# Kernel tuning notes

Hardware: AMD Instinct MI355X
Metric: run time of the kernel (lower is better)

## Reference

```python
import jax, jax.numpy as jnp
import numpy as np

S = 8192   # seq_len (== max_seq_len)
K = 4096   # in_features
N = 4096   # out_features


def setup_inputs() -> dict:
    key = jax.random.key(0)
    k1, k2, k3, k4, k5 = jax.random.split(key, 5)
    # symmetric int8 activations and weights in [-127, 127]
    x = jax.random.randint(k1, (S, K), -127, 128, dtype=jnp.int32).astype(jnp.int8)
    weight_q = jax.random.randint(k2, (N, K), -127, 128, dtype=jnp.int32).astype(jnp.int8)
    # positive dequant scales (per-row symmetric quant: scale = absmax/127)
    scale_x = jax.random.uniform(k3, (S,), minval=0.5, maxval=2.0, dtype=jnp.float32) / 127.0
    scale_w = jax.random.uniform(k4, (N,), minval=0.5, maxval=2.0, dtype=jnp.float32) / 127.0
    # per-output-row requantization scale from the MinMax observer
    scale_y = jax.random.uniform(k5, (S,), minval=0.5, maxval=2.0, dtype=jnp.float32)
    return {"x": x, "weight_q": weight_q, "scale_x": scale_x,
            "scale_w": scale_w, "scale_y": scale_y}


def reference(x, weight_q, scale_x, scale_w, scale_y):
    # int8 GEMM with int32 accumulation: acc[s, n] = sum_k x[s, k] * w[n, k]
    acc = jnp.matmul(x.astype(jnp.int32), weight_q.T.astype(jnp.int32))  # [S, N] int32
    # fused three-scale dequant + requant: (acc * sx[s] * sw[n]) / sy[s]
    scale = (scale_x / scale_y)[:, None] * scale_w[None, :]               # [S, N]
    out_f = acc.astype(jnp.float32) * scale
    out_q = jnp.clip(jnp.round(out_f), -128.0, 127.0).astype(jnp.int8)    # int8 output
    return out_q, scale_y
```

## Files before the change

kernel.cpp:

```cpp
#include <hip/hip_runtime.h>
#include <stdint.h>

#define S_DIM 8192
#define K_DIM 4096
#define N_DIM 4096

#define BM 128
#define BN 128
#define BK 128

typedef int v4i __attribute__((ext_vector_type(4)));

__global__ void pack_i8(const int* __restrict__ src, int* __restrict__ dst,
                        int n4) {
    int i = blockIdx.x * blockDim.x + threadIdx.x;
    if (i >= n4) return;
    int4 a = ((const int4*)src)[i];
    dst[i] = (a.x & 0xFF) | ((a.y & 0xFF) << 8) | ((a.z & 0xFF) << 16)
           | ((a.w & 0xFF) << 24);
}

__global__ void copy_sy(const float* __restrict__ sy, float* __restrict__ out) {
    int i = blockIdx.x * blockDim.x + threadIdx.x;
    if (i < S_DIM) out[(size_t)S_DIM * N_DIM + i] = sy[i];
}

__device__ __forceinline__ void g2lds16(const void* g, void* l) {
    __builtin_amdgcn_global_load_lds((const __attribute__((address_space(1))) void*)g,
                                     (__attribute__((address_space(3))) void*)l,
                                     16, 0, 0);
}

__launch_bounds__(256)
__global__ void gemm_i8(const signed char* __restrict__ xp,
                        const signed char* __restrict__ wp,
                        const float* __restrict__ sx,
                        const float* __restrict__ sw,
                        const float* __restrict__ sy,
                        float* __restrict__ out) {
    __shared__ __align__(16) signed char As[BM * BK];
    __shared__ __align__(16) signed char Bs[BN * BK];

    const int tid  = threadIdx.x;
    const int lane = tid & 63;
    const int quad = lane >> 4;
    const int l16  = lane & 15;
    const int wave = tid >> 6;
    const int wm = wave >> 1;
    const int wn = wave & 1;
    const int bn = blockIdx.x;
    const int bm = blockIdx.y;

    const signed char* aG = xp + (size_t)(bm * BM) * K_DIM;
    const signed char* bG = wp + (size_t)(bn * BN) * K_DIM;

    const int csw = l16 & 7;

    v4i acc[4][4];
#pragma unroll
    for (int i = 0; i < 4; i++)
#pragma unroll
        for (int j = 0; j < 4; j++) acc[i][j] = 0;

    for (int kk = 0; kk < K_DIM; kk += BK) {
        __syncthreads();
#pragma unroll
        for (int i = 0; i < 4; i++) {
            int li  = i * 256 + tid;
            int row = li >> 3;
            int c   = li & 7;
            int g   = c ^ (row & 7);
            g2lds16(aG + (size_t)row * K_DIM + kk + (g << 4), As + li * 16);
            g2lds16(bG + (size_t)row * K_DIM + kk + (g << 4), Bs + li * 16);
        }
        __syncthreads();

#pragma unroll
        for (int ks = 0; ks < 2; ks++) {
            const int slot = ((ks << 2) | quad);
            v4i af[4], bf[4];
#pragma unroll
            for (int t = 0; t < 4; t++) {
                af[t] = *(const v4i*)(As + (wm * 64 + t * 16 + l16) * BK
                                         + ((slot ^ csw) << 4));
                bf[t] = *(const v4i*)(Bs + (wn * 64 + t * 16 + l16) * BK
                                         + ((slot ^ csw) << 4));
            }
#pragma unroll
            for (int mt = 0; mt < 4; mt++)
#pragma unroll
                for (int nt = 0; nt < 4; nt++)
                    acc[mt][nt] = __builtin_amdgcn_mfma_i32_16x16x64_i8(
                        af[mt], bf[nt], acc[mt][nt], 0, 0, 0);
        }
    }

    const int s_base = bm * BM + wm * 64;
    const int n_base = bn * BN + wn * 64;
#pragma unroll
    for (int mt = 0; mt < 4; mt++) {
#pragma unroll
        for (int r = 0; r < 4; r++) {
            int s = s_base + mt * 16 + quad * 4 + r;
            float rs = sx[s] / sy[s];
            float* orow = out + (size_t)s * N_DIM;
#pragma unroll
            for (int nt = 0; nt < 4; nt++) {
                int n = n_base + nt * 16 + l16;
                float v = rintf((float)acc[mt][nt][r] * (rs * sw[n]));
                v = fminf(fmaxf(v, -128.f), 127.f);
                orow[n] = v;
            }
        }
    }
}

__global__ void gemm_naive(const int* __restrict__ x, const int* __restrict__ w,
                           const float* __restrict__ sx, const float* __restrict__ sw,
                           const float* __restrict__ sy, float* __restrict__ out) {
    int n = blockIdx.x * blockDim.x + threadIdx.x;
    int s = blockIdx.y;
    const int4* xr = (const int4*)(x + (size_t)s * K_DIM);
    const int4* wr = (const int4*)(w + (size_t)n * K_DIM);
    int acc = 0;
    for (int k = 0; k < K_DIM / 4; k++) {
        int4 a = xr[k], b = wr[k];
        acc += a.x * b.x + a.y * b.y + a.z * b.z + a.w * b.w;
    }
    float v = rintf((float)acc * (sx[s] / sy[s] * sw[n]));
    out[(size_t)s * N_DIM + n] = fminf(fmaxf(v, -128.f), 127.f);
}

extern "C" void kernel_launch(void* const* d_in, const int* in_sizes, int n_in,
                              void* d_out, int out_size, void* d_ws, size_t ws_size,
                              hipStream_t stream) {
    const int*   x  = (const int*)d_in[0];
    const int*   wq = (const int*)d_in[1];
    const float* sx = (const float*)d_in[2];
    const float* sw = (const float*)d_in[3];
    const float* sy = (const float*)d_in[4];
    float* out = (float*)d_out;

    copy_sy<<<dim3((S_DIM + 255) / 256), dim3(256), 0, stream>>>(sy, out);

    const size_t need = (size_t)S_DIM * K_DIM + (size_t)N_DIM * K_DIM;
    if (ws_size >= need) {
        signed char* xp = (signed char*)d_ws;
        signed char* wp = xp + (size_t)S_DIM * K_DIM;
        pack_i8<<<dim3(S_DIM * K_DIM / 4 / 256), dim3(256), 0, stream>>>(
            x, (int*)xp, S_DIM * K_DIM / 4);
        pack_i8<<<dim3(N_DIM * K_DIM / 4 / 256), dim3(256), 0, stream>>>(
            wq, (int*)wp, N_DIM * K_DIM / 4);
        gemm_i8<<<dim3(N_DIM / BN, S_DIM / BM), dim3(256), 0, stream>>>(
            xp, wp, sx, sw, sy, out);
    } else {
        gemm_naive<<<dim3(N_DIM / 256, S_DIM), dim3(256), 0, stream>>>(
            x, wq, sx, sw, sy, out);
    }
}
```

Measured before the change: 424.1 us.

## Widen GEMM tile to 128x256 and fuse pack/copy prep kernels into one launch

```diff
diff --git a/kernel.cpp b/kernel.cpp
--- a/kernel.cpp
+++ b/kernel.cpp
@@ -6,18 +6,29 @@
 #define N_DIM 4096
 
 #define BM 128
-#define BN 128
+#define BN 256
 #define BK 128
 
 typedef int v4i __attribute__((ext_vector_type(4)));
 
-__global__ void pack_i8(const int* __restrict__ src, int* __restrict__ dst,
-                        int n4) {
-    int i = blockIdx.x * blockDim.x + threadIdx.x;
-    if (i >= n4) return;
-    int4 a = ((const int4*)src)[i];
-    dst[i] = (a.x & 0xFF) | ((a.y & 0xFF) << 8) | ((a.z & 0xFF) << 16)
-           | ((a.w & 0xFF) << 24);
+__global__ void prep(const int* __restrict__ x, const int* __restrict__ w,
+                     const float* __restrict__ sy,
+                     int* __restrict__ dst, float* __restrict__ out) {
+    const int nx = S_DIM * K_DIM / 4;
+    const int nw = N_DIM * K_DIM / 4;
+    int i = blockIdx.x * 256 + threadIdx.x;
+    if (i < nx) {
+        int4 a = ((const int4*)x)[i];
+        dst[i] = (a.x & 0xFF) | ((a.y & 0xFF) << 8) | ((a.z & 0xFF) << 16)
+               | ((a.w & 0xFF) << 24);
+    } else if (i < nx + nw) {
+        int4 a = ((const int4*)w)[i - nx];
+        dst[i] = (a.x & 0xFF) | ((a.y & 0xFF) << 8) | ((a.z & 0xFF) << 16)
+               | ((a.w & 0xFF) << 24);
+    } else {
+        int j = i - nx - nw;
+        if (j < S_DIM) out[(size_t)S_DIM * N_DIM + j] = sy[j];
+    }
 }
 
 __global__ void copy_sy(const float* __restrict__ sy, float* __restrict__ out) {
@@ -31,7 +42,7 @@
                                      16, 0, 0);
 }
 
-__launch_bounds__(256)
+__launch_bounds__(256, 2)
 __global__ void gemm_i8(const signed char* __restrict__ xp,
                         const signed char* __restrict__ wp,
                         const float* __restrict__ sx,
@@ -56,47 +67,59 @@
 
     const int csw = l16 & 7;
 
-    v4i acc[4][4];
+    int aOff[4], bOff[8];
+#pragma unroll
+    for (int i = 0; i < 4; i++) {
+        int li = i * 256 + tid;
+        int row = li >> 3, c = li & 7, g = c ^ (row & 7);
+        aOff[i] = row * K_DIM + (g << 4);
+    }
+#pragma unroll
+    for (int i = 0; i < 8; i++) {
+        int li = i * 256 + tid;
+        int row = li >> 3, c = li & 7, g = c ^ (row & 7);
+        bOff[i] = row * K_DIM + (g << 4);
+    }
+
+    v4i acc[4][8];
 #pragma unroll
     for (int i = 0; i < 4; i++)
 #pragma unroll
-        for (int j = 0; j < 4; j++) acc[i][j] = 0;
+        for (int j = 0; j < 8; j++) acc[i][j] = 0;
 
     for (int kk = 0; kk < K_DIM; kk += BK) {
         __syncthreads();
 #pragma unroll
-        for (int i = 0; i < 4; i++) {
-            int li  = i * 256 + tid;
-            int row = li >> 3;
-            int c   = li & 7;
-            int g   = c ^ (row & 7);
-            g2lds16(aG + (size_t)row * K_DIM + kk + (g << 4), As + li * 16);
-            g2lds16(bG + (size_t)row * K_DIM + kk + (g << 4), Bs + li * 16);
-        }
+        for (int i = 0; i < 4; i++)
+            g2lds16(aG + aOff[i] + kk, As + (i * 256 + tid) * 16);
+#pragma unroll
+        for (int i = 0; i < 8; i++)
+            g2lds16(bG + bOff[i] + kk, Bs + (i * 256 + tid) * 16);
         __syncthreads();
 
 #pragma unroll
         for (int ks = 0; ks < 2; ks++) {
-            const int slot = ((ks << 2) | quad);
-            v4i af[4], bf[4];
+            const int slot = ((ks << 2) | quad) ^ csw;
+            v4i af[4], bf[8];
 #pragma unroll
-            for (int t = 0; t < 4; t++) {
+            for (int t = 0; t < 4; t++)
                 af[t] = *(const v4i*)(As + (wm * 64 + t * 16 + l16) * BK
-                                         + ((slot ^ csw) << 4));
-                bf[t] = *(const v4i*)(Bs + (wn * 64 + t * 16 + l16) * BK
-                                         + ((slot ^ csw) << 4));
-            }
+                                         + (slot << 4));
+#pragma unroll
+            for (int u = 0; u < 8; u++)
+                bf[u] = *(const v4i*)(Bs + (wn * 128 + u * 16 + l16) * BK
+                                         + (slot << 4));
 #pragma unroll
             for (int mt = 0; mt < 4; mt++)
 #pragma unroll
-                for (int nt = 0; nt < 4; nt++)
+                for (int nt = 0; nt < 8; nt++)
                     acc[mt][nt] = __builtin_amdgcn_mfma_i32_16x16x64_i8(
                         af[mt], bf[nt], acc[mt][nt], 0, 0, 0);
         }
     }
 
     const int s_base = bm * BM + wm * 64;
-    const int n_base = bn * BN + wn * 64;
+    const int n_base = bn * BN + wn * 128;
 #pragma unroll
     for (int mt = 0; mt < 4; mt++) {
 #pragma unroll
@@ -105,7 +128,7 @@
             float rs = sx[s] / sy[s];
             float* orow = out + (size_t)s * N_DIM;
 #pragma unroll
-            for (int nt = 0; nt < 4; nt++) {
+            for (int nt = 0; nt < 8; nt++) {
                 int n = n_base + nt * 16 + l16;
                 float v = rintf((float)acc[mt][nt][r] * (rs * sw[n]));
                 v = fminf(fmaxf(v, -128.f), 127.f);
@@ -141,19 +164,17 @@
     const float* sy = (const float*)d_in[4];
     float* out = (float*)d_out;
 
-    copy_sy<<<dim3((S_DIM + 255) / 256), dim3(256), 0, stream>>>(sy, out);
-
     const size_t need = (size_t)S_DIM * K_DIM + (size_t)N_DIM * K_DIM;
     if (ws_size >= need) {
         signed char* xp = (signed char*)d_ws;
         signed char* wp = xp + (size_t)S_DIM * K_DIM;
-        pack_i8<<<dim3(S_DIM * K_DIM / 4 / 256), dim3(256), 0, stream>>>(
-            x, (int*)xp, S_DIM * K_DIM / 4);
-        pack_i8<<<dim3(N_DIM * K_DIM / 4 / 256), dim3(256), 0, stream>>>(
-            wq, (int*)wp, N_DIM * K_DIM / 4);
+        const int nprep = (S_DIM * K_DIM / 4) + (N_DIM * K_DIM / 4) + S_DIM;
+        prep<<<dim3((nprep + 255) / 256), dim3(256), 0, stream>>>(
+            x, wq, sy, (int*)xp, out);
         gemm_i8<<<dim3(N_DIM / BN, S_DIM / BM), dim3(256), 0, stream>>>(
             xp, wp, sx, sw, sy, out);
     } else {
+        copy_sy<<<dim3((S_DIM + 255) / 256), dim3(256), 0, stream>>>(sy, out);
         gemm_naive<<<dim3(N_DIM / 256, S_DIM), dim3(256), 0, stream>>>(
             x, wq, sx, sw, sy, out);
     }
```

New measurement: 391.5 us. 1.08x faster.
